# Performance work log

Hardware: AMD Instinct MI355X
Metric: run time of the kernel (lower is better)

## Reference

```python
import jax, jax.numpy as jnp
import numpy as np

B, N, E = 64, 1024, 16384
ZH, EF_DIM = 128, 64
RUP, RMAX, P = 10.0, 10.0, 6
MAX_ZVOCAB = 13   # max of z_embedding_dim=[13,4,8,6,6,8,2,4]
MAX_EFVOCAB = 8   # max of edge_features_embedding_dim=[6,3,3,8]


def setup_inputs() -> dict:
    key = jax.random.key(0)
    ks = jax.random.split(key, 9)
    z = jax.random.randint(ks[0], (B, N, 8), 0, 2)
    pos = jax.random.normal(ks[1], (B, N, 3), dtype=jnp.float32)
    idx_u = jax.random.randint(ks[2], (B, E), 0, N)
    # guarantee u != v so edge length > 0 almost surely
    idx_v = (idx_u + jax.random.randint(ks[3], (B, E), 1, N)) % N
    edge_index = jnp.stack([idx_u, idx_v], axis=1)  # (B,2,E)
    edge_features = jax.random.randint(ks[4], (B, E, 4), 0, 3)
    center_pos = jax.random.normal(ks[5], (B, N, 3), dtype=jnp.float32)
    # embedding tables padded to max vocab (unused rows never indexed)
    z_tables = jax.random.normal(ks[6], (8, MAX_ZVOCAB, ZH), dtype=jnp.float32)
    ef_tables = jax.random.normal(ks[7], (4, MAX_EFVOCAB, EF_DIM), dtype=jnp.float32)
    dV_table = jax.random.normal(ks[8], (3, EF_DIM), dtype=jnp.float32)
    return dict(z=z, pos=pos, edge_index=edge_index, edge_features=edge_features,
                center_pos=center_pos, z_tables=z_tables, ef_tables=ef_tables,
                dV_table=dV_table)


def _gather_nodes(x, idx):
    # x: (B,N,D), idx: (B,E) -> (B,E,D)
    return jnp.take_along_axis(x, idx[..., None], axis=1)


def reference(z, pos, edge_index, edge_features, center_pos, z_tables, ef_tables, dV_table):
    # node embedding: z_emb[0] + sum_{i=2..6} z_emb[i] (indices 1 and 7 unused, per source)
    emb1 = z_tables[0][z[..., 0]]
    for i in range(2, 7):
        emb1 = emb1 + z_tables[i][z[..., i]]

    idx_u, idx_v = edge_index[:, 0], edge_index[:, 1]
    posu = _gather_nodes(pos, idx_u)           # (B,E,3)
    posv = _gather_nodes(pos, idx_v)
    ev = posu - posv
    el = jnp.sqrt(jnp.maximum(jnp.sum(ev * ev, axis=-1, keepdims=True), 1e-24))  # (B,E,1)

    # Gaussian RBF over [0, rbound_upper]
    offsets = jnp.linspace(0.0, RUP, EF_DIM, dtype=jnp.float32)
    coeff = -0.5 / (offsets[1] - offsets[0]) ** 2
    ef = jnp.exp(coeff * (el - offsets) ** 2)  # (B,E,EF_DIM)

    for i in range(4):
        ef = ef + ef_tables[i][edge_features[..., i]]

    # dV sign branch (center_pos provided)
    center_pad = _gather_nodes(center_pos, idx_v)
    ecross = jnp.cross(posu, posv)
    dV = jnp.sum(ecross * center_pad, axis=-1)            # (B,E)
    dV_sign = jnp.sign(dV).astype(jnp.int32) + 1          # in {0,1,2}
    ef = ef * dV_table[dV_sign]

    # smooth polynomial envelope (DimeNet-style), zero beyond r_max
    x = el / RMAX
    env = (1.0 - 0.5 * (P + 1) * (P + 2) * x ** P
           + P * (P + 2) * x ** (P + 1)
           - 0.5 * P * (P + 1) * x ** (P + 2))
    env = jnp.where(x < 1.0, env, 0.0)
    ef = ef * env
    return emb1, ef
```

## Files before the change

kernel.cpp:

```cpp
#include <hip/hip_runtime.h>

#define BATCH   64
#define NNODE   1024
#define NEDGE   16384
#define ZHDIM   128
#define EFDIM   64
#define MAXZV   13
#define MAXEFV  8

__global__ __launch_bounds__(256) void emb1_kernel(
    const int*   __restrict__ z,
    const float* __restrict__ z_tables,
    float*       __restrict__ out)
{
    int tid  = blockIdx.x * 256 + threadIdx.x;
    int node = tid >> 5;
    int c4   = tid & 31;
    if (node >= BATCH * NNODE) return;

    const int* zp = z + node * 8;
    int i0 = zp[0];
    int i2 = zp[2], i3 = zp[3], i4 = zp[4], i5 = zp[5], i6 = zp[6];

    const float4* t = (const float4*)z_tables;
    float4 a0 = t[(0 * MAXZV + i0) * 32 + c4];
    float4 a2 = t[(2 * MAXZV + i2) * 32 + c4];
    float4 a3 = t[(3 * MAXZV + i3) * 32 + c4];
    float4 a4 = t[(4 * MAXZV + i4) * 32 + c4];
    float4 a5 = t[(5 * MAXZV + i5) * 32 + c4];
    float4 a6 = t[(6 * MAXZV + i6) * 32 + c4];

    float4 s;
    s.x = a0.x + a2.x + a3.x + a4.x + a5.x + a6.x;
    s.y = a0.y + a2.y + a3.y + a4.y + a5.y + a6.y;
    s.z = a0.z + a2.z + a3.z + a4.z + a5.z + a6.z;
    s.w = a0.w + a2.w + a3.w + a4.w + a5.w + a6.w;

    ((float4*)out)[node * 32 + c4] = s;
}

__global__ __launch_bounds__(256) void ef_kernel(
    const float* __restrict__ pos,
    const int*   __restrict__ edge_index,
    const int*   __restrict__ edge_features,
    const float* __restrict__ center_pos,
    const float* __restrict__ ef_tables,
    const float* __restrict__ dV_table,
    float*       __restrict__ out)
{
    int tid  = blockIdx.x * 256 + threadIdx.x;
    int edge = tid >> 4;
    int c4   = tid & 15;
    if (edge >= BATCH * NEDGE) return;

    int b = edge >> 14;
    int e = edge & (NEDGE - 1);

    int iu = edge_index[(b * 2 + 0) * NEDGE + e];
    int iv = edge_index[(b * 2 + 1) * NEDGE + e];

    const float* pu = pos + (size_t)(b * NNODE + iu) * 3;
    const float* pv = pos + (size_t)(b * NNODE + iv) * 3;
    float ux = pu[0], uy = pu[1], uz = pu[2];
    float vx = pv[0], vy = pv[1], vz = pv[2];

    float dx = ux - vx, dy = uy - vy, dz = uz - vz;
    float el = sqrtf(fmaxf(dx * dx + dy * dy + dz * dz, 1e-24f));

    float cx = uy * vz - uz * vy;
    float cy = uz * vx - ux * vz;
    float cz = ux * vy - uy * vx;
    const float* cp = center_pos + (size_t)(b * NNODE + iv) * 3;
    float dV = cx * cp[0] + cy * cp[1] + cz * cp[2];
    int sgn = (dV > 0.0f) ? 2 : ((dV < 0.0f) ? 0 : 1);

    float x  = el * 0.1f;
    float x2 = x * x;
    float x3 = x2 * x;
    float x6 = x3 * x3;
    float x7 = x6 * x;
    float x8 = x7 * x;
    float env = 1.0f - 28.0f * x6 + 48.0f * x7 - 21.0f * x8;
    env = (x < 1.0f) ? env : 0.0f;

    const int* efp = edge_features + (size_t)edge * 4;
    int f0 = efp[0], f1 = efp[1], f2 = efp[2], f3 = efp[3];
    float4 t0 = ((const float4*)(ef_tables + (size_t)(0 * MAXEFV + f0) * EFDIM))[c4];
    float4 t1 = ((const float4*)(ef_tables + (size_t)(1 * MAXEFV + f1) * EFDIM))[c4];
    float4 t2 = ((const float4*)(ef_tables + (size_t)(2 * MAXEFV + f2) * EFDIM))[c4];
    float4 t3 = ((const float4*)(ef_tables + (size_t)(3 * MAXEFV + f3) * EFDIM))[c4];
    float4 dvt = ((const float4*)(dV_table + (size_t)sgn * EFDIM))[c4];

    const float step  = 10.0f / 63.0f;
    const float coeff = -0.5f / (step * step);

    float4 res;
    {
        float tsum[4] = {t0.x + t1.x + t2.x + t3.x,
                         t0.y + t1.y + t2.y + t3.y,
                         t0.z + t1.z + t2.z + t3.z,
                         t0.w + t1.w + t2.w + t3.w};
        float dvv[4] = {dvt.x, dvt.y, dvt.z, dvt.w};
        float r[4];
#pragma unroll
        for (int k = 0; k < 4; ++k) {
            int j = c4 * 4 + k;
            float off = step * (float)j;
            float d = el - off;
            float g = expf(coeff * d * d);
            r[k] = (g + tsum[k]) * dvv[k] * env;
        }
        res.x = r[0]; res.y = r[1]; res.z = r[2]; res.w = r[3];
    }

    ((float4*)out)[(size_t)edge * 16 + c4] = res;
}

extern "C" void kernel_launch(void* const* d_in, const int* in_sizes, int n_in,
                              void* d_out, int out_size, void* d_ws, size_t ws_size,
                              hipStream_t stream) {
    const int*   z             = (const int*)  d_in[0];
    const float* pos           = (const float*)d_in[1];
    const int*   edge_index    = (const int*)  d_in[2];
    const int*   edge_features = (const int*)  d_in[3];
    const float* center_pos    = (const float*)d_in[4];
    const float* z_tables      = (const float*)d_in[5];
    const float* ef_tables     = (const float*)d_in[6];
    const float* dV_table      = (const float*)d_in[7];

    float* out_emb1 = (float*)d_out;
    float* out_ef   = out_emb1 + (size_t)BATCH * NNODE * ZHDIM;

    {
        int threads = BATCH * NNODE * 32;
        emb1_kernel<<<threads / 256, 256, 0, stream>>>(z, z_tables, out_emb1);
    }
    {
        int threads = BATCH * NEDGE * 16;
        ef_kernel<<<threads / 256, 256, 0, stream>>>(
            pos, edge_index, edge_features, center_pos, ef_tables, dV_table, out_ef);
    }
}
```

Measured before the change: 414.5 us.

## Precombine edge-feature tables with dV scaling and split per-edge scalar pass

Builds a table in workspace holding (sum of four edge-feature embeddings) times dV row for all 4096x3 combos. A separate per-edge kernel computes length, envelope, sign and row id once per edge instead of sixteen times, and the expand kernel then does one table gather plus the RBF. This removes the redundant per-lane scalar math and the four-table gather. It adds two launches and a workspace round trip for the per-edge scalars.

Result: faster. 354.7 us (-14.4%).

```diff
diff --git a/kernel.cpp b/kernel.cpp
--- a/kernel.cpp
+++ b/kernel.cpp
@@ -7,6 +7,124 @@
 #define EFDIM   64
 #define MAXZV   13
 #define MAXEFV  8
+#define NEDGES_TOT (BATCH * NEDGE)
+#define NCOMBO  4096
+#define AROWS   (NCOMBO * 3)
+
+#define WS_A_OFF_FLOATS      0
+#define WS_SCAL_OFF_FLOATS   (1024 * 1024)
+
+__global__ __launch_bounds__(256) void combine_tables_kernel(
+    const float* __restrict__ ef_tables,
+    const float* __restrict__ dV_table,
+    float*       __restrict__ A)
+{
+    int tid = blockIdx.x * 256 + threadIdx.x;
+    int row = tid >> 4;
+    int c4  = tid & 15;
+    int combo = row / 3;
+    int s     = row - combo * 3;
+    int f3 = combo & 7, f2 = (combo >> 3) & 7, f1 = (combo >> 6) & 7, f0 = (combo >> 9) & 7;
+
+    const float4* T = (const float4*)ef_tables;
+    float4 t0 = T[(0 * MAXEFV + f0) * 16 + c4];
+    float4 t1 = T[(1 * MAXEFV + f1) * 16 + c4];
+    float4 t2 = T[(2 * MAXEFV + f2) * 16 + c4];
+    float4 t3 = T[(3 * MAXEFV + f3) * 16 + c4];
+    float4 dv = ((const float4*)dV_table)[s * 16 + c4];
+
+    float4 o;
+    o.x = (t0.x + t1.x + t2.x + t3.x) * dv.x;
+    o.y = (t0.y + t1.y + t2.y + t3.y) * dv.y;
+    o.z = (t0.z + t1.z + t2.z + t3.z) * dv.z;
+    o.w = (t0.w + t1.w + t2.w + t3.w) * dv.w;
+    ((float4*)A)[row * 16 + c4] = o;
+}
+
+__global__ __launch_bounds__(256) void edge_scalar_kernel(
+    const float* __restrict__ pos,
+    const int*   __restrict__ edge_index,
+    const int*   __restrict__ edge_features,
+    const float* __restrict__ center_pos,
+    float4*      __restrict__ scal)
+{
+    int edge = blockIdx.x * 256 + threadIdx.x;
+    int b = edge >> 14;
+    int e = edge & (NEDGE - 1);
+
+    int iu = edge_index[(b * 2 + 0) * NEDGE + e];
+    int iv = edge_index[(b * 2 + 1) * NEDGE + e];
+
+    const float* pu = pos + (size_t)(b * NNODE + iu) * 3;
+    const float* pv = pos + (size_t)(b * NNODE + iv) * 3;
+    float ux = pu[0], uy = pu[1], uz = pu[2];
+    float vx = pv[0], vy = pv[1], vz = pv[2];
+
+    float dx = ux - vx, dy = uy - vy, dz = uz - vz;
+    float el = sqrtf(fmaxf(dx * dx + dy * dy + dz * dz, 1e-24f));
+
+    float cx = uy * vz - uz * vy;
+    float cy = uz * vx - ux * vz;
+    float cz = ux * vy - uy * vx;
+    const float* cp = center_pos + (size_t)(b * NNODE + iv) * 3;
+    float dV = cx * cp[0] + cy * cp[1] + cz * cp[2];
+    int sgn = (dV > 0.0f) ? 2 : ((dV < 0.0f) ? 0 : 1);
+
+    float x  = el * 0.1f;
+    float x3 = x * x * x;
+    float x6 = x3 * x3;
+    float env = 1.0f - 28.0f * x6 + 48.0f * x6 * x - 21.0f * x6 * x * x;
+    env = (x < 1.0f) ? env : 0.0f;
+
+    int4 f = ((const int4*)edge_features)[edge];
+    int combo = ((f.x * 8 + f.y) * 8 + f.z) * 8 + f.w;
+    int rowid = combo * 3 + sgn;
+
+    float4 o;
+    o.x = el;
+    o.y = env;
+    o.z = __int_as_float(rowid);
+    o.w = __int_as_float(sgn);
+    scal[edge] = o;
+}
+
+__global__ __launch_bounds__(256) void ef_expand_kernel(
+    const float4* __restrict__ scal,
+    const float*  __restrict__ A,
+    const float*  __restrict__ dV_table,
+    float*        __restrict__ out)
+{
+    int tid  = blockIdx.x * 256 + threadIdx.x;
+    int edge = tid >> 4;
+    int c4   = tid & 15;
+
+    float4 sc = scal[edge];
+    float el  = sc.x;
+    float env = sc.y;
+    int rowid = __float_as_int(sc.z);
+    int sgn   = __float_as_int(sc.w);
+
+    float4 a  = ((const float4*)A)[rowid * 16 + c4];
+    float4 dv = ((const float4*)dV_table)[sgn * 16 + c4];
+
+    const float step  = 10.0f / 63.0f;
+    const float coeff = -0.5f / (step * step);
+
+    float av[4]  = {a.x, a.y, a.z, a.w};
+    float dvv[4] = {dv.x, dv.y, dv.z, dv.w};
+    float r[4];
+#pragma unroll
+    for (int k = 0; k < 4; ++k) {
+        int j = c4 * 4 + k;
+        float d = el - step * (float)j;
+        float g = expf(coeff * d * d);
+        r[k] = fmaf(g, dvv[k], av[k]) * env;
+    }
+
+    float4 res;
+    res.x = r[0]; res.y = r[1]; res.z = r[2]; res.w = r[3];
+    ((float4*)out)[(size_t)edge * 16 + c4] = res;
+}
 
 __global__ __launch_bounds__(256) void emb1_kernel(
     const int*   __restrict__ z,
@@ -16,7 +134,6 @@
     int tid  = blockIdx.x * 256 + threadIdx.x;
     int node = tid >> 5;
     int c4   = tid & 31;
-    if (node >= BATCH * NNODE) return;
 
     const int* zp = z + node * 8;
     int i0 = zp[0];
@@ -39,83 +156,6 @@
     ((float4*)out)[node * 32 + c4] = s;
 }
 
-__global__ __launch_bounds__(256) void ef_kernel(
-    const float* __restrict__ pos,
-    const int*   __restrict__ edge_index,
-    const int*   __restrict__ edge_features,
-    const float* __restrict__ center_pos,
-    const float* __restrict__ ef_tables,
-    const float* __restrict__ dV_table,
-    float*       __restrict__ out)
-{
-    int tid  = blockIdx.x * 256 + threadIdx.x;
-    int edge = tid >> 4;
-    int c4   = tid & 15;
-    if (edge >= BATCH * NEDGE) return;
-
-    int b = edge >> 14;
-    int e = edge & (NEDGE - 1);
-
-    int iu = edge_index[(b * 2 + 0) * NEDGE + e];
-    int iv = edge_index[(b * 2 + 1) * NEDGE + e];
-
-    const float* pu = pos + (size_t)(b * NNODE + iu) * 3;
-    const float* pv = pos + (size_t)(b * NNODE + iv) * 3;
-    float ux = pu[0], uy = pu[1], uz = pu[2];
-    float vx = pv[0], vy = pv[1], vz = pv[2];
-
-    float dx = ux - vx, dy = uy - vy, dz = uz - vz;
-    float el = sqrtf(fmaxf(dx * dx + dy * dy + dz * dz, 1e-24f));
-
-    float cx = uy * vz - uz * vy;
-    float cy = uz * vx - ux * vz;
-    float cz = ux * vy - uy * vx;
-    const float* cp = center_pos + (size_t)(b * NNODE + iv) * 3;
-    float dV = cx * cp[0] + cy * cp[1] + cz * cp[2];
-    int sgn = (dV > 0.0f) ? 2 : ((dV < 0.0f) ? 0 : 1);
-
-    float x  = el * 0.1f;
-    float x2 = x * x;
-    float x3 = x2 * x;
-    float x6 = x3 * x3;
-    float x7 = x6 * x;
-    float x8 = x7 * x;
-    float env = 1.0f - 28.0f * x6 + 48.0f * x7 - 21.0f * x8;
-    env = (x < 1.0f) ? env : 0.0f;
-
-    const int* efp = edge_features + (size_t)edge * 4;
-    int f0 = efp[0], f1 = efp[1], f2 = efp[2], f3 = efp[3];
-    float4 t0 = ((const float4*)(ef_tables + (size_t)(0 * MAXEFV + f0) * EFDIM))[c4];
-    float4 t1 = ((const float4*)(ef_tables + (size_t)(1 * MAXEFV + f1) * EFDIM))[c4];
-    float4 t2 = ((const float4*)(ef_tables + (size_t)(2 * MAXEFV + f2) * EFDIM))[c4];
-    float4 t3 = ((const float4*)(ef_tables + (size_t)(3 * MAXEFV + f3) * EFDIM))[c4];
-    float4 dvt = ((const float4*)(dV_table + (size_t)sgn * EFDIM))[c4];
-
-    const float step  = 10.0f / 63.0f;
-    const float coeff = -0.5f / (step * step);
-
-    float4 res;
-    {
-        float tsum[4] = {t0.x + t1.x + t2.x + t3.x,
-                         t0.y + t1.y + t2.y + t3.y,
-                         t0.z + t1.z + t2.z + t3.z,
-                         t0.w + t1.w + t2.w + t3.w};
-        float dvv[4] = {dvt.x, dvt.y, dvt.z, dvt.w};
-        float r[4];
-#pragma unroll
-        for (int k = 0; k < 4; ++k) {
-            int j = c4 * 4 + k;
-            float off = step * (float)j;
-            float d = el - off;
-            float g = expf(coeff * d * d);
-            r[k] = (g + tsum[k]) * dvv[k] * env;
-        }
-        res.x = r[0]; res.y = r[1]; res.z = r[2]; res.w = r[3];
-    }
-
-    ((float4*)out)[(size_t)edge * 16 + c4] = res;
-}
-
 extern "C" void kernel_launch(void* const* d_in, const int* in_sizes, int n_in,
                               void* d_out, int out_size, void* d_ws, size_t ws_size,
                               hipStream_t stream) {
@@ -131,13 +171,16 @@
     float* out_emb1 = (float*)d_out;
     float* out_ef   = out_emb1 + (size_t)BATCH * NNODE * ZHDIM;
 
-    {
-        int threads = BATCH * NNODE * 32;
-        emb1_kernel<<<threads / 256, 256, 0, stream>>>(z, z_tables, out_emb1);
-    }
-    {
-        int threads = BATCH * NEDGE * 16;
-        ef_kernel<<<threads / 256, 256, 0, stream>>>(
-            pos, edge_index, edge_features, center_pos, ef_tables, dV_table, out_ef);
-    }
+    float*  ws_A    = (float*)d_ws + WS_A_OFF_FLOATS;
+    float4* ws_scal = (float4*)((float*)d_ws + WS_SCAL_OFF_FLOATS);
+
+    combine_tables_kernel<<<AROWS * 16 / 256, 256, 0, stream>>>(ef_tables, dV_table, ws_A);
+
+    edge_scalar_kernel<<<NEDGES_TOT / 256, 256, 0, stream>>>(
+        pos, edge_index, edge_features, center_pos, ws_scal);
+
+    emb1_kernel<<<BATCH * NNODE * 32 / 256, 256, 0, stream>>>(z, z_tables, out_emb1);
+
+    ef_expand_kernel<<<NEDGES_TOT * 16 / 256, 256, 0, stream>>>(
+        ws_scal, ws_A, dV_table, out_ef);
 }
```
